# Kernel optimization log

Hardware: AMD Instinct MI355X
Metric: run time of the kernel (lower is better)

The kernel has to match this reference:

```python
import jax, jax.numpy as jnp
import numpy as np

N_NODES = 50000
N_EDGES = 600000
N_RELS = 19
D_IN = 128
D_HID = 64
D_OUT = 2


def setup_inputs() -> dict:
    key = jax.random.key(0)
    ks = jax.random.split(key, 10)
    feat = jax.random.normal(ks[0], (N_NODES, D_IN), dtype=jnp.float32)
    src = jax.random.randint(ks[1], (N_EDGES,), 0, N_NODES)
    dst = jax.random.randint(ks[2], (N_EDGES,), 0, N_NODES)
    etype = jax.random.randint(ks[3], (N_EDGES,), 0, N_RELS)
    s1 = 1.0 / np.sqrt(D_IN)
    s2 = 1.0 / np.sqrt(D_HID)
    W1 = jax.random.normal(ks[4], (N_RELS, D_IN, D_HID), dtype=jnp.float32) * s1
    loop1 = jax.random.normal(ks[5], (D_IN, D_HID), dtype=jnp.float32) * s1
    b1 = jnp.zeros((D_HID,), dtype=jnp.float32)
    W2 = jax.random.normal(ks[6], (N_RELS, D_HID, D_OUT), dtype=jnp.float32) * s2
    loop2 = jax.random.normal(ks[7], (D_HID, D_OUT), dtype=jnp.float32) * s2
    b2 = jnp.zeros((D_OUT,), dtype=jnp.float32)
    return {"feat": feat, "W1": W1, "loop1": loop1, "b1": b1,
            "W2": W2, "loop2": loop2, "b2": b2,
            "src": src, "dst": dst, "etype": etype}


def _rel_graph_conv(h, W, loop_w, bias, src, dst, etype, activation):
    # Per-relation transform of all nodes: [N, R, O]; then gather per edge.
    # (num_rels * out_feat is small, so this is cheaper than gathering W per edge.)
    transformed = jnp.einsum('nd,rdo->nro', h, W)
    msg = transformed[src, etype]                      # [E, O] edge messages
    agg = jax.ops.segment_sum(msg, dst, num_segments=h.shape[0])  # scatter-add
    out = agg + h @ loop_w + bias                      # self-loop + bias
    if activation is not None:
        out = activation(out)
    return out


def reference(feat, W1, loop1, b1, W2, loop2, b2, src, dst, etype):
    h = _rel_graph_conv(feat, W1, loop1, b1, src, dst, etype, jax.nn.relu)
    h = _rel_graph_conv(h, W2, loop2, b2, src, dst, etype, None)
    return h
```

## Files before the change

### kernel.cpp

```cpp
#include <hip/hip_runtime.h>

#define N_NODES 50000
#define N_EDGES 600000
#define N_RELS  19
#define D_IN    128
#define D_HID   64
#define D_OUT   2
#define EDGE_TILES ((N_EDGES + 127) / 128 + N_RELS)
#define SL_BLOCKS  ((N_NODES + 63) / 64)

typedef unsigned short u16;
typedef unsigned int   u32;
typedef __attribute__((ext_vector_type(8))) short sfrag;
typedef __attribute__((ext_vector_type(4))) float f32x4;

__device__ __forceinline__ u16 f2bf(float f){
  union { float f; u32 i; } v; v.f = f;
  u32 r = v.i + 0x7fffu + ((v.i >> 16) & 1u);
  return (u16)(r >> 16);
}
__device__ __forceinline__ float bf2f(u16 u){
  union { u32 i; float f; } v; v.i = ((u32)u) << 16; return v.f;
}

__global__ void k_prep(const float* __restrict__ W1, const float* __restrict__ loop1,
                       const float* __restrict__ W2, const float* __restrict__ loop2,
                       u16* __restrict__ W1Tb, u16* __restrict__ loop1Tb,
                       u16* __restrict__ W2T2b, int* __restrict__ hist_rel,
                       int* __restrict__ hist_dst, int* __restrict__ gcnt){
  int idx = blockIdx.x * 256 + threadIdx.x;
  if (idx < N_RELS)  hist_rel[idx] = 0;
  if (idx < N_NODES) hist_dst[idx] = 0;
  if (idx == 0) gcnt[0] = 0;
  const int T1 = N_RELS * D_HID * D_IN;
  const int T2 = T1 + 48 * D_HID;
  const int T3 = T2 + D_HID * D_IN;
  if (idx < T1) {
    int r = idx / (D_HID * D_IN);
    int t = idx - r * (D_HID * D_IN);
    int j = t >> 7, d = t & 127;
    W1Tb[idx] = f2bf(W1[(r * D_IN + d) * D_HID + j]);
  } else if (idx < T2) {
    int k2 = idx - T1;
    int j = k2 >> 6, d = k2 & 63;
    float v = 0.f;
    if (j < 2 * N_RELS)       v = W2[((j >> 1) * D_HID + d) * D_OUT + (j & 1)];
    else if (j < 2 * N_RELS + 2) v = loop2[d * D_OUT + (j - 2 * N_RELS)];
    W2T2b[k2] = f2bf(v);
  } else if (idx < T3) {
    int k2 = idx - T2;
    int j = k2 >> 7, d = k2 & 127;
    loop1Tb[k2] = f2bf(loop1[d * D_HID + j]);
  }
}

__global__ __launch_bounds__(256) void k_fused_pre(const float* __restrict__ feat,
                                                   u16* __restrict__ featb,
                                                   const int* __restrict__ et,
                                                   const int* __restrict__ dst,
                                                   int* __restrict__ hist_rel,
                                                   int* __restrict__ hist_dst){
  int i = blockIdx.x * 256 + threadIdx.x;
  float2 f = ((const float2*)feat)[i];
  ((u32*)featb)[i] = (u32)f2bf(f.x) | ((u32)f2bf(f.y) << 16);
  if (blockIdx.x < (N_EDGES + 255) / 256) {
    __shared__ int lh[N_RELS];
    int tid = threadIdx.x;
    if (tid < N_RELS) lh[tid] = 0;
    __syncthreads();
    int e = blockIdx.x * 256 + tid;
    if (e < N_EDGES) {
      atomicAdd(&lh[et[e]], 1);
      atomicAdd(&hist_dst[dst[e]], 1);
    }
    __syncthreads();
    if (tid < N_RELS && lh[tid]) atomicAdd(&hist_rel[tid], lh[tid]);
  }
}

__global__ __launch_bounds__(256) void k_alloc_scan(
    const int* __restrict__ hist_dst, int* __restrict__ dstart,
    int* __restrict__ cur_dst, int* __restrict__ gcnt,
    const int* __restrict__ hist_rel, int* __restrict__ offs,
    int* __restrict__ toff, int* __restrict__ cur_rel){
  if (blockIdx.x == 196) {
    if (threadIdx.x == 0) {
      int acc = 0, tacc = 0;
      offs[0] = 0; toff[0] = 0;
      for (int r = 0; r < N_RELS; ++r) {
        cur_rel[r] = acc;
        int c = hist_rel[r];
        acc += c;                offs[r + 1] = acc;
        tacc += (c + 127) >> 7;  toff[r + 1] = tacc;
      }
    }
    return;
  }
  __shared__ int wbase[4];
  int tid = threadIdx.x, lane = tid & 63, wv = tid >> 6;
  int n = blockIdx.x * 256 + tid;
  int v = (n < N_NODES) ? hist_dst[n] : 0;
  int x = v;
  #pragma unroll
  for (int o = 1; o < 64; o <<= 1) { int u = __shfl_up(x, o); if (lane >= o) x += u; }
  if (lane == 63) wbase[wv] = atomicAdd(gcnt, x);
  __syncthreads();
  int start = wbase[wv] + x - v;
  if (n < N_NODES) { dstart[n] = start; cur_dst[n] = start; }
}

__global__ __launch_bounds__(256) void k_scatter_rel(const int* __restrict__ et,
                                                     int* __restrict__ cursor,
                                                     int* __restrict__ perm){
  __shared__ int lh[N_RELS], base[N_RELS];
  int tid = threadIdx.x;
  if (tid < N_RELS) lh[tid] = 0;
  __syncthreads();
  int e = blockIdx.x * 256 + tid;
  int r = 0, my = 0;
  bool valid = e < N_EDGES;
  if (valid) { r = et[e]; my = atomicAdd(&lh[r], 1); }
  __syncthreads();
  if (tid < N_RELS && lh[tid]) base[tid] = atomicAdd(&cursor[tid], lh[tid]);
  __syncthreads();
  if (valid) perm[base[r] + my] = e;
}

__global__ __launch_bounds__(256) void k_se1(
    const u16* __restrict__ featb, const u16* __restrict__ W1Tb,
    const u16* __restrict__ loop1Tb, const float* __restrict__ b1,
    const int* __restrict__ src, const int* __restrict__ dst,
    const int* __restrict__ perm, const int* __restrict__ offs,
    const int* __restrict__ toff, int* __restrict__ cur_dst,
    u16* __restrict__ msgbuf, float* __restrict__ agg1f){
  __shared__ __align__(16) u16 Als[128][136];
  __shared__ __align__(16) u16 Bls[64][136];
  __shared__ int posIds[128];
  int tid = threadIdx.x, lane = tid & 63, w = tid >> 6;
  int r16 = lane & 15, c4 = lane >> 4;

  if (blockIdx.x >= EDGE_TILES) {
    int base = (blockIdx.x - EDGE_TILES) * 64;
    { int j = tid >> 2, seg = tid & 3;
      const uint4* g = (const uint4*)(loop1Tb + j * 128) + seg * 4;
      uint4* d = (uint4*)&Bls[j][seg * 32];
      d[0] = g[0]; d[1] = g[1]; d[2] = g[2]; d[3] = g[3]; }
    { int i = tid >> 2, seg = tid & 3;
      int n = base + i; if (n >= N_NODES) n = N_NODES - 1;
      const uint4* g = (const uint4*)(featb + (size_t)n * D_IN) + seg * 4;
      uint4* d = (uint4*)&Als[i][seg * 32];
      d[0] = g[0]; d[1] = g[1]; d[2] = g[2]; d[3] = g[3]; }
    __syncthreads();
    sfrag aF[4];
    #pragma unroll
    for (int kk = 0; kk < 4; ++kk)
      aF[kk] = *(const sfrag*)&Als[w * 16 + r16][kk * 32 + c4 * 8];
    #pragma unroll
    for (int ct = 0; ct < 4; ++ct) {
      f32x4 acc = {0.f, 0.f, 0.f, 0.f};
      #pragma unroll
      for (int kk = 0; kk < 4; ++kk) {
        sfrag bF = *(const sfrag*)&Bls[ct * 16 + r16][kk * 32 + c4 * 8];
        acc = __builtin_amdgcn_mfma_f32_16x16x32_bf16(aF[kk], bF, acc, 0, 0, 0);
      }
      int col = ct * 16 + r16;
      float bias = b1[col];
      #pragma unroll
      for (int reg = 0; reg < 4; ++reg) {
        int row = base + w * 16 + c4 * 4 + reg;
        if (row < N_NODES) agg1f[(size_t)row * D_HID + col] = acc[reg] + bias;
      }
    }
    return;
  }

  int b = blockIdx.x;
  unsigned long long mm = __ballot((lane < N_RELS) && (b >= toff[lane + 1]));
  int rel = __popcll(mm);
  if (rel >= N_RELS) return;
  int ts = offs[rel] + ((b - toff[rel]) << 7);
  int vc = offs[rel + 1] - ts; if (vc > 128) vc = 128;

  {
    int j = tid >> 2, seg = tid & 3;
    const uint4* g = (const uint4*)(W1Tb + ((size_t)rel * 64 + j) * 128) + seg * 4;
    uint4* d = (uint4*)&Bls[j][seg * 32];
    d[0] = g[0]; d[1] = g[1]; d[2] = g[2]; d[3] = g[3];
  }
  #pragma unroll
  for (int p = 0; p < 2; ++p) {
    int i = p * 64 + (tid >> 2), seg = tid & 3;
    if (i < vc) {
      int e = perm[ts + i];
      if (seg == 0) posIds[i] = atomicAdd(&cur_dst[dst[e]], 1);
      const uint4* g = (const uint4*)(featb + (size_t)src[e] * D_IN) + seg * 4;
      uint4* d = (uint4*)&Als[i][seg * 32];
      d[0] = g[0]; d[1] = g[1]; d[2] = g[2]; d[3] = g[3];
    } else if (seg == 0) posIds[i] = -1;
  }
  __syncthreads();

  sfrag aF[2][4];
  #pragma unroll
  for (int mt = 0; mt < 2; ++mt)
    #pragma unroll
    for (int kk = 0; kk < 4; ++kk)
      aF[mt][kk] = *(const sfrag*)&Als[w * 32 + mt * 16 + r16][kk * 32 + c4 * 8];
  f32x4 accAll[2][4];
  #pragma unroll
  for (int ct = 0; ct < 4; ++ct) {
    sfrag bF[4];
    #pragma unroll
    for (int kk = 0; kk < 4; ++kk)
      bF[kk] = *(const sfrag*)&Bls[ct * 16 + r16][kk * 32 + c4 * 8];
    #pragma unroll
    for (int mt = 0; mt < 2; ++mt) {
      f32x4 acc = {0.f, 0.f, 0.f, 0.f};
      #pragma unroll
      for (int kk = 0; kk < 4; ++kk)
        acc = __builtin_amdgcn_mfma_f32_16x16x32_bf16(aF[mt][kk], bF[kk], acc, 0, 0, 0);
      accAll[mt][ct] = acc;
    }
  }
  float* msg = (float*)&Als[0][0];
  #pragma unroll
  for (int mt = 0; mt < 2; ++mt)
    #pragma unroll
    for (int ct = 0; ct < 4; ++ct) {
      int col = ct * 16 + r16;
      #pragma unroll
      for (int reg = 0; reg < 4; ++reg) {
        int row = w * 32 + mt * 16 + c4 * 4 + reg;
        msg[row * 68 + col] = accAll[mt][ct][reg];
      }
    }
  __syncthreads();
  { int row = tid >> 1, half = tid & 1;
    int pos = posIds[row];
    if (pos >= 0) {
      const float* mr = msg + row * 68 + half * 32;
      u32 pk[16];
      #pragma unroll
      for (int q = 0; q < 16; ++q)
        pk[q] = (u32)f2bf(mr[2 * q]) | ((u32)f2bf(mr[2 * q + 1]) << 16);
      uint4* d = (uint4*)(msgbuf + (size_t)pos * D_HID + half * 32);
      d[0] = *(uint4*)&pk[0];  d[1] = *(uint4*)&pk[4];
      d[2] = *(uint4*)&pk[8];  d[3] = *(uint4*)&pk[12];
    } }
}

__global__ __launch_bounds__(256) void k_agg_t(
    const u16* __restrict__ msgbuf, const int* __restrict__ dstart,
    const int* __restrict__ cnt, const float* __restrict__ agg1f,
    const u16* __restrict__ W2T2b, const float* __restrict__ b2,
    float* __restrict__ Tmat, float* __restrict__ out){
  __shared__ __align__(16) u16 Hls[64][72];
  __shared__ __align__(16) u16 Bls[48][72];
  int tid = threadIdx.x, lane = tid & 63, w = tid >> 6;
  int n0 = blockIdx.x * 64;
  #pragma unroll
  for (int p = 0; p < 2; ++p) {
    int idx = p * 256 + tid;
    if (idx < 384) ((uint4*)&Bls[idx >> 3][0])[idx & 7] = ((const uint4*)W2T2b)[idx];
  }
  int h = lane >> 5, c = lane & 31;
  for (int t = 0; t < 16; ++t) {
    int i = w * 16 + t, n = n0 + i;
    float a0 = 0.f, a1 = 0.f;
    if (n < N_NODES) {
      int s = dstart[n], epos = s + cnt[n];
      for (int q = s + h; q < epos; q += 2) {
        u32 v = ((const u32*)msgbuf)[(size_t)q * 32 + c];
        a0 += bf2f((u16)(v & 0xffffu));
        a1 += bf2f((u16)(v >> 16));
      }
    }
    a0 += __shfl_down(a0, 32);
    a1 += __shfl_down(a1, 32);
    if (h == 0) {
      u32 pk = 0;
      if (n < N_NODES) {
        float2 sl = ((const float2*)(agg1f + (size_t)n * D_HID))[c];
        float v0 = a0 + sl.x, v1 = a1 + sl.y;
        v0 = v0 > 0.f ? v0 : 0.f;
        v1 = v1 > 0.f ? v1 : 0.f;
        pk = (u32)f2bf(v0) | ((u32)f2bf(v1) << 16);
      }
      *(u32*)&Hls[i][2 * c] = pk;
    }
  }
  __syncthreads();
  int r16 = lane & 15, c4 = lane >> 4;
  sfrag aF[2];
  aF[0] = *(const sfrag*)&Hls[w * 16 + r16][c4 * 8];
  aF[1] = *(const sfrag*)&Hls[w * 16 + r16][32 + c4 * 8];
  #pragma unroll
  for (int ct = 0; ct < 3; ++ct) {
    f32x4 acc = {0.f, 0.f, 0.f, 0.f};
    #pragma unroll
    for (int kk = 0; kk < 2; ++kk) {
      sfrag bF = *(const sfrag*)&Bls[ct * 16 + r16][kk * 32 + c4 * 8];
      acc = __builtin_amdgcn_mfma_f32_16x16x32_bf16(aF[kk], bF, acc, 0, 0, 0);
    }
    int col = ct * 16 + r16;
    #pragma unroll
    for (int reg = 0; reg < 4; ++reg) {
      int row = w * 16 + c4 * 4 + reg;
      int n = n0 + row;
      if (n < N_NODES && col < 40) {
        float v = acc[reg];
        Tmat[(size_t)n * 40 + col] = v;
        if (col >= 38) out[n * 2 + (col - 38)] = v + b2[col - 38];
      }
    }
  }
}

__global__ __launch_bounds__(256) void k_edge2s(const int* __restrict__ src,
                                                const int* __restrict__ dst,
                                                const int* __restrict__ et,
                                                const float* __restrict__ Tmat,
                                                float* __restrict__ out){
  int e = blockIdx.x * 256 + threadIdx.x;
  if (e < N_EDGES) {
    int s = src[e], d = dst[e], r = et[e];
    float2 tv = *(const float2*)(Tmat + (size_t)s * 40 + 2 * r);
    atomicAdd(&out[d * 2],     tv.x);
    atomicAdd(&out[d * 2 + 1], tv.y);
  }
}

extern "C" void kernel_launch(void* const* d_in, const int* in_sizes, int n_in,
                              void* d_out, int out_size, void* d_ws, size_t ws_size,
                              hipStream_t stream){
  const float* feat  = (const float*)d_in[0];
  const float* W1    = (const float*)d_in[1];
  const float* loop1 = (const float*)d_in[2];
  const float* b1    = (const float*)d_in[3];
  const float* W2    = (const float*)d_in[4];
  const float* loop2 = (const float*)d_in[5];
  const float* b2    = (const float*)d_in[6];
  const int* src     = (const int*)d_in[7];
  const int* dst     = (const int*)d_in[8];
  const int* et      = (const int*)d_in[9];
  float* out = (float*)d_out;

  char* w = (char*)d_ws;
  u16*   W1Tb     = (u16*)(w);
  u16*   W2T2b    = (u16*)(w + 311296);
  u16*   loop1Tb  = (u16*)(w + 317440);
  int*   hist_rel = (int*)(w + 333824);
  int*   offs     = (int*)(w + 333952);
  int*   toff     = (int*)(w + 334080);
  int*   cur_rel  = (int*)(w + 334208);
  int*   gcnt     = (int*)(w + 334336);
  int*   hist_dst = (int*)(w + 334464);
  int*   dstart   = (int*)(w + 534464);
  int*   cur_dst  = (int*)(w + 734464);
  int*   perm     = (int*)(w + 934464);
  u16*   featb    = (u16*)(w + 3334464);
  float* agg1f    = (float*)(w + 16134464);
  float* Tmat     = (float*)(w + 28934464);
  u16*   msgbuf   = (u16*)(w + 36934464);

  k_prep       <<<652,   256, 0, stream>>>(W1, loop1, W2, loop2, W1Tb, loop1Tb, W2T2b,
                                           hist_rel, hist_dst, gcnt);
  k_fused_pre  <<<12500, 256, 0, stream>>>(feat, featb, et, dst, hist_rel, hist_dst);
  k_alloc_scan <<<197,   256, 0, stream>>>(hist_dst, dstart, cur_dst, gcnt,
                                           hist_rel, offs, toff, cur_rel);
  k_scatter_rel<<<2344,  256, 0, stream>>>(et, cur_rel, perm);
  k_se1        <<<EDGE_TILES + SL_BLOCKS, 256, 0, stream>>>(
                   featb, W1Tb, loop1Tb, b1, src, dst, perm, offs, toff,
                   cur_dst, msgbuf, agg1f);
  k_agg_t      <<<SL_BLOCKS, 256, 0, stream>>>(msgbuf, dstart, hist_dst, agg1f,
                                               W2T2b, b2, Tmat, out);
  k_edge2s     <<<2344,  256, 0, stream>>>(src, dst, et, Tmat, out);
}
```

Measured before the change: 373.1 us.

## Assign one wavefront per node in aggregation and replace MFMA with shuffle dot products

The aggregation kernel now gives each wavefront a single destination node, launching 12500 blocks of four nodes instead of 782 blocks of 64 nodes that each looped over 16 nodes per wave. The layer-2 transform is done with wave shuffles against bf16 weights in padded LDS, replacing the MFMA tile. The aim is more parallelism and memory-level concurrency in the latency-bound gather. The cost is repeated weight loads per block and a 32-step shuffle loop per node. Some other edits are cosmetic.

```diff
diff --git a/kernel.cpp b/kernel.cpp
--- a/kernel.cpp
+++ b/kernel.cpp
@@ -44,7 +44,7 @@
     int k2 = idx - T1;
     int j = k2 >> 6, d = k2 & 63;
     float v = 0.f;
-    if (j < 2 * N_RELS)       v = W2[((j >> 1) * D_HID + d) * D_OUT + (j & 1)];
+    if (j < 2 * N_RELS)          v = W2[((j >> 1) * D_HID + d) * D_OUT + (j & 1)];
     else if (j < 2 * N_RELS + 2) v = loop2[d * D_OUT + (j - 2 * N_RELS)];
     W2T2b[k2] = f2bf(v);
   } else if (idx < T3) {
@@ -249,70 +249,47 @@
     } }
 }
 
-__global__ __launch_bounds__(256) void k_agg_t(
+__global__ __launch_bounds__(256) void k_agg_T(
     const u16* __restrict__ msgbuf, const int* __restrict__ dstart,
     const int* __restrict__ cnt, const float* __restrict__ agg1f,
     const u16* __restrict__ W2T2b, const float* __restrict__ b2,
     float* __restrict__ Tmat, float* __restrict__ out){
-  __shared__ __align__(16) u16 Hls[64][72];
-  __shared__ __align__(16) u16 Bls[48][72];
-  int tid = threadIdx.x, lane = tid & 63, w = tid >> 6;
-  int n0 = blockIdx.x * 64;
-  #pragma unroll
-  for (int p = 0; p < 2; ++p) {
+  __shared__ u32 Wls[48 * 33];
+  int tid = threadIdx.x, wv = tid >> 6, lane = tid & 63;
+  #pragma unroll
+  for (int p = 0; p < 6; ++p) {
     int idx = p * 256 + tid;
-    if (idx < 384) ((uint4*)&Bls[idx >> 3][0])[idx & 7] = ((const uint4*)W2T2b)[idx];
-  }
+    Wls[(idx >> 5) * 33 + (idx & 31)] = ((const u32*)W2T2b)[idx];
+  }
+  int n = blockIdx.x * 4 + wv;
+  int s = dstart[n], epos = s + cnt[n];
   int h = lane >> 5, c = lane & 31;
-  for (int t = 0; t < 16; ++t) {
-    int i = w * 16 + t, n = n0 + i;
-    float a0 = 0.f, a1 = 0.f;
-    if (n < N_NODES) {
-      int s = dstart[n], epos = s + cnt[n];
-      for (int q = s + h; q < epos; q += 2) {
-        u32 v = ((const u32*)msgbuf)[(size_t)q * 32 + c];
-        a0 += bf2f((u16)(v & 0xffffu));
-        a1 += bf2f((u16)(v >> 16));
-      }
-    }
-    a0 += __shfl_down(a0, 32);
-    a1 += __shfl_down(a1, 32);
-    if (h == 0) {
-      u32 pk = 0;
-      if (n < N_NODES) {
-        float2 sl = ((const float2*)(agg1f + (size_t)n * D_HID))[c];
-        float v0 = a0 + sl.x, v1 = a1 + sl.y;
-        v0 = v0 > 0.f ? v0 : 0.f;
-        v1 = v1 > 0.f ? v1 : 0.f;
-        pk = (u32)f2bf(v0) | ((u32)f2bf(v1) << 16);
-      }
-      *(u32*)&Hls[i][2 * c] = pk;
-    }
-  }
-  __syncthreads();
-  int r16 = lane & 15, c4 = lane >> 4;
-  sfrag aF[2];
-  aF[0] = *(const sfrag*)&Hls[w * 16 + r16][c4 * 8];
-  aF[1] = *(const sfrag*)&Hls[w * 16 + r16][32 + c4 * 8];
-  #pragma unroll
-  for (int ct = 0; ct < 3; ++ct) {
-    f32x4 acc = {0.f, 0.f, 0.f, 0.f};
-    #pragma unroll
-    for (int kk = 0; kk < 2; ++kk) {
-      sfrag bF = *(const sfrag*)&Bls[ct * 16 + r16][kk * 32 + c4 * 8];
-      acc = __builtin_amdgcn_mfma_f32_16x16x32_bf16(aF[kk], bF, acc, 0, 0, 0);
-    }
-    int col = ct * 16 + r16;
-    #pragma unroll
-    for (int reg = 0; reg < 4; ++reg) {
-      int row = w * 16 + c4 * 4 + reg;
-      int n = n0 + row;
-      if (n < N_NODES && col < 40) {
-        float v = acc[reg];
-        Tmat[(size_t)n * 40 + col] = v;
-        if (col >= 38) out[n * 2 + (col - 38)] = v + b2[col - 38];
-      }
-    }
+  float a0 = 0.f, a1 = 0.f;
+  for (int i = s + h; i < epos; i += 2) {
+    u32 v = ((const u32*)msgbuf)[(size_t)i * 32 + c];
+    a0 += bf2f((u16)(v & 0xffffu));
+    a1 += bf2f((u16)(v >> 16));
+  }
+  a0 += __shfl_down(a0, 32);
+  a1 += __shfl_down(a1, 32);
+  float2 sl = ((const float2*)(agg1f + (size_t)n * D_HID))[c];
+  float v0 = a0 + sl.x, v1 = a1 + sl.y;
+  v0 = v0 > 0.f ? v0 : 0.f;
+  v1 = v1 > 0.f ? v1 : 0.f;
+  __syncthreads();
+  int row = lane < 48 ? lane : 0;
+  const u32* wr = &Wls[row * 33];
+  float acc = 0.f;
+  #pragma unroll
+  for (int q = 0; q < 32; ++q) {
+    float h0  = __shfl(v0, q);
+    float h1v = __shfl(v1, q);
+    u32 wp = wr[q];
+    acc += h0 * bf2f((u16)(wp & 0xffffu)) + h1v * bf2f((u16)(wp >> 16));
+  }
+  if (lane < 40) {
+    Tmat[(size_t)n * 40 + lane] = acc;
+    if (lane >= 38) out[n * 2 + (lane - 38)] = acc + b2[lane - 38];
   }
 }
 
@@ -323,8 +300,8 @@
                                                 float* __restrict__ out){
   int e = blockIdx.x * 256 + threadIdx.x;
   if (e < N_EDGES) {
-    int s = src[e], d = dst[e], r = et[e];
-    float2 tv = *(const float2*)(Tmat + (size_t)s * 40 + 2 * r);
+    float2 tv = *(const float2*)(Tmat + (size_t)src[e] * 40 + 2 * et[e]);
+    int d = dst[e];
     atomicAdd(&out[d * 2],     tv.x);
     atomicAdd(&out[d * 2 + 1], tv.y);
   }
@@ -372,7 +349,7 @@
   k_se1        <<<EDGE_TILES + SL_BLOCKS, 256, 0, stream>>>(
                    featb, W1Tb, loop1Tb, b1, src, dst, perm, offs, toff,
                    cur_dst, msgbuf, agg1f);
-  k_agg_t      <<<SL_BLOCKS, 256, 0, stream>>>(msgbuf, dstart, hist_dst, agg1f,
-                                               W2T2b, b2, Tmat, out);
+  k_agg_T      <<<12500, 256, 0, stream>>>(msgbuf, dstart, hist_dst, agg1f,
+                                           W2T2b, b2, Tmat, out);
   k_edge2s     <<<2344,  256, 0, stream>>>(src, dst, et, Tmat, out);
 }
```

After: 377.5 us. No clear change (+1.2%).
